# Kernel optimization log

Hardware: AMD Instinct MI355X
Metric: run time of the kernel (lower is better)

Reference implementation:

```python
import jax, jax.numpy as jnp
import numpy as np

B, C = 2, 128
FMAP_HW = [(256, 256), (128, 128), (64, 64), (32, 32)]
N_ROIS = 4000
POOL = (7, 7)
N_ANCH = 300000
N_POS = 1000          # anchors with match > 0 (class 1)
N_NEG = 200000        # anchors with match == -1
SHEM_POOLSIZE = 20
N_CLASSES = 2


def setup_inputs() -> dict:
    key = jax.random.key(0)
    ks = jax.random.split(key, 10)
    inp = {}
    for l, (h, w) in enumerate(FMAP_HW):
        inp[f"fmap{l}"] = jax.random.normal(ks[l], (B, C, h, w), dtype=jnp.float32)
    # rois: normalized (y1, x1, y2, x2, batch_ix)
    ctr = jax.random.uniform(ks[4], (N_ROIS, 2))
    sz = jax.random.uniform(ks[5], (N_ROIS, 2), minval=0.02, maxval=0.5)
    lo = jnp.clip(ctr - sz / 2, 0.0, 1.0)
    hi = jnp.clip(ctr + sz / 2, 0.0, 1.0)
    bix = jax.random.randint(ks[6], (N_ROIS, 1), 0, B).astype(jnp.float32)
    inp["rois"] = jnp.concatenate([lo, hi, bix], axis=1)
    # fixed layout for static shapes: [pos | neg | neutral]
    am = np.zeros(N_ANCH, np.int32)
    am[:N_POS] = 1
    am[N_POS:N_POS + N_NEG] = -1
    inp["anchor_matches"] = jnp.asarray(am)
    inp["class_pred_logits"] = jax.random.normal(ks[7], (N_ANCH, N_CLASSES), dtype=jnp.float32)
    inp["pred_deltas"] = jax.random.normal(ks[8], (N_ANCH, 4), dtype=jnp.float32) * 0.1
    inp["target_deltas"] = jax.random.normal(ks[9], (N_ANCH, 4), dtype=jnp.float32) * 0.1
    return inp


def _roi_align_2d(fmap, boxes, batch_ix, pool):
    """Bilinear ROI align, one sample at each bin center.
    fmap: [B,C,H,W]; boxes: [N,4] in fmap pixel coords (y1,x1,y2,x2).
    Returns [N,C,ph,pw]."""
    Hc, Wc = fmap.shape[2], fmap.shape[3]
    ph, pw = pool
    y1, x1, y2, x2 = boxes[:, 0], boxes[:, 1], boxes[:, 2], boxes[:, 3]
    bh = (y2 - y1) / ph
    bw = (x2 - x1) / pw
    iy = jnp.arange(ph, dtype=jnp.float32) + 0.5
    ix = jnp.arange(pw, dtype=jnp.float32) + 0.5
    sy = jnp.clip(y1[:, None] + bh[:, None] * iy[None, :], 0.0, Hc - 1.0)  # [N,ph]
    sx = jnp.clip(x1[:, None] + bw[:, None] * ix[None, :], 0.0, Wc - 1.0)  # [N,pw]
    y0f = jnp.floor(sy)
    x0f = jnp.floor(sx)
    y0 = y0f.astype(jnp.int32)
    x0 = x0f.astype(jnp.int32)
    y1i = jnp.minimum(y0 + 1, Hc - 1)
    x1i = jnp.minimum(x0 + 1, Wc - 1)
    wy = (sy - y0f)[:, :, None, None]  # [N,ph,1,1]
    wx = (sx - x0f)[:, None, :, None]  # [N,1,pw,1]
    b = batch_ix[:, None, None]

    def gather(yy, xx):
        # yy [N,ph], xx [N,pw] -> [N,ph,pw,C]
        return fmap[b, :, yy[:, :, None], xx[:, None, :]]

    v00 = gather(y0, x0)
    v01 = gather(y0, x1i)
    v10 = gather(y1i, x0)
    v11 = gather(y1i, x1i)
    out = (v00 * (1 - wy) * (1 - wx) + v01 * (1 - wy) * wx
           + v10 * wy * (1 - wx) + v11 * wy * wx)
    return jnp.transpose(out, (0, 3, 1, 2))


def _forward(fmaps, rois, anchor_matches, class_pred_logits, pred_deltas, target_deltas):
    boxes = rois[:, :4]
    batch_ix = rois[:, 4].astype(jnp.int32)
    h = boxes[:, 2] - boxes[:, 0]
    w = boxes[:, 3] - boxes[:, 1]
    roi_level = jnp.clip(
        jnp.round(4.0 + jnp.log2(jnp.sqrt(h * w + 1e-12))).astype(jnp.int32), 0, 3)
    boxes_sg = jax.lax.stop_gradient(boxes)  # original detaches level_boxes
    pooled = jnp.zeros((N_ROIS, C, POOL[0], POOL[1]), fmaps[0].dtype)
    for lvl, f in enumerate(fmaps):
        He, We = f.shape[2], f.shape[3]
        lb = boxes_sg * jnp.array([He, We, He, We], jnp.float32)
        pl = _roi_align_2d(f, lb, batch_ix, POOL)
        mask = (roi_level == lvl).astype(pl.dtype)[:, None, None, None]
        pooled = pooled + mask * pl  # each roi hits exactly one level; order preserved

    # ---- class loss with SHEM (layout: [:N_POS] pos, [N_POS:N_POS+N_NEG] neg) ----
    pos_logits = class_pred_logits[:N_POS]
    pos_targets = anchor_matches[:N_POS].astype(jnp.int32)
    pos_logp = jax.nn.log_softmax(pos_logits, axis=1)
    pos_loss = -jnp.mean(jnp.take_along_axis(pos_logp, pos_targets[:, None], axis=1))

    neg_logits = class_pred_logits[N_POS:N_POS + N_NEG]
    neg_bg_prob = jax.nn.softmax(neg_logits, axis=1)[:, 0]
    negative_count = N_POS  # max(1, n_pos)
    pool_n = min(negative_count * SHEM_POOLSIZE, N_NEG)
    order = jnp.argsort(neg_bg_prob)          # ascending bg prob = hardest first
    pool_idx = order[:pool_n]
    perm = jax.random.permutation(jax.random.key(1), pool_n)
    neg_ix = pool_idx[perm[:negative_count]]  # stochastic draw from hard pool
    neg_loss = -jnp.mean(jax.nn.log_softmax(neg_logits[neg_ix], axis=1)[:, 0])
    class_loss = (pos_loss + neg_loss) / 2.0

    # ---- bbox smooth-L1 on positives (beta=1, mean reduction) ----
    diff = jnp.abs(pred_deltas[:N_POS] - target_deltas[:N_POS])
    sl1 = jnp.where(diff < 1.0, 0.5 * diff * diff, diff - 0.5)
    bbox_loss = jnp.mean(sl1)
    return pooled, class_loss, bbox_loss


def reference(fmap0, fmap1, fmap2, fmap3, rois, anchor_matches,
              class_pred_logits, pred_deltas, target_deltas):
    return _forward([fmap0, fmap1, fmap2, fmap3], rois, anchor_matches,
                    class_pred_logits, pred_deltas, target_deltas)
```

## Files before the change

### kernel.cpp

```cpp
#include <hip/hip_runtime.h>
#include <hip/hip_bf16.h>
#include <cstdint>

#define NROIS  4000
#define NCH    128
#define NBINS  49
#define N_POSA 1000
#define N_NEGA 200000
#define POOLN  20000
#define HBITS_A 13
#define ABINS  8192
#define PBINS  4096
#define SUBN   4096
#define NTRBLK 2720
#define NPREP  106
#define NRANKA 512
#define NRANKP 40
#define TPAD   136

#define L0OFF 0ull
#define L1OFF 16777216ull
#define L2OFF 20971520ull
#define L3OFF 22020096ull
#define TLELEMS 22282240ull

__device__ __forceinline__ uint32_t rotl32d(uint32_t v, int r) { return (v << r) | (v >> (32-r)); }

__device__ void tf2x32(uint32_t k0, uint32_t k1, uint32_t& x0, uint32_t& x1)
{
    const uint32_t ks2 = k0 ^ k1 ^ 0x1BD11BDAu;
    const int R0[4] = {13,15,26,6};
    const int R1[4] = {17,29,16,24};
    x0 += k0; x1 += k1;
#pragma unroll
    for (int r = 0; r < 4; ++r) { x0 += x1; x1 = rotl32d(x1, R0[r]); x1 ^= x0; }
    x0 += k1;  x1 += ks2 + 1u;
#pragma unroll
    for (int r = 0; r < 4; ++r) { x0 += x1; x1 = rotl32d(x1, R1[r]); x1 ^= x0; }
    x0 += ks2; x1 += k0 + 2u;
#pragma unroll
    for (int r = 0; r < 4; ++r) { x0 += x1; x1 = rotl32d(x1, R0[r]); x1 ^= x0; }
    x0 += k0;  x1 += k1 + 3u;
#pragma unroll
    for (int r = 0; r < 4; ++r) { x0 += x1; x1 = rotl32d(x1, R1[r]); x1 ^= x0; }
    x0 += k1;  x1 += ks2 + 4u;
#pragma unroll
    for (int r = 0; r < 4; ++r) { x0 += x1; x1 = rotl32d(x1, R0[r]); x1 ^= x0; }
    x0 += ks2; x1 += k0 + 5u;
}

__device__ __forceinline__ unsigned int monobits(float x) {
    unsigned int u = __float_as_uint(x);
    return (u & 0x80000000u) ? ~u : (u | 0x80000000u);
}

__device__ __forceinline__ unsigned short f2bf(float x) {
    union { __hip_bfloat16 h; unsigned short u; } c;
    c.h = __float2bfloat16(x);
    return c.u;
}

__global__ void k_zero(unsigned int* __restrict__ h)
{
    h[blockIdx.x*256 + threadIdx.x] = 0u;
}

__global__ __launch_bounds__(256) void k_trprep(
    const float* __restrict__ f0, const float* __restrict__ f1,
    const float* __restrict__ f2, const float* __restrict__ f3,
    __hip_bfloat16* __restrict__ tl,
    unsigned long long* __restrict__ T1, unsigned long long* __restrict__ T2,
    unsigned int* __restrict__ histA,
    unsigned int* __restrict__ histP1, unsigned int* __restrict__ histP2,
    const int* __restrict__ am, const float* __restrict__ logits,
    const float* __restrict__ pd, const float* __restrict__ td,
    float* __restrict__ prt, int ntr)
{
    __shared__ __align__(16) unsigned char smraw[32768];
    const int bid = blockIdx.x;
    const int t   = threadIdx.x;

    if (bid < ntr) {
        unsigned short* s = (unsigned short*)smraw;
        const int bz = bid / 1360;
        const int r  = bid - bz*1360;
        int lvl, tile;
        if      (r < 1024) { lvl = 0; tile = r; }
        else if (r < 1280) { lvl = 1; tile = r - 1024; }
        else if (r < 1344) { lvl = 2; tile = r - 1280; }
        else               { lvl = 3; tile = r - 1344; }
        const int HW = 65536 >> (2*lvl);
        const float* in = (lvl==0) ? f0 : (lvl==1) ? f1 : (lvl==2) ? f2 : f3;
        const size_t ooff = (lvl==0) ? L0OFF : (lvl==1) ? L1OFF : (lvl==2) ? L2OFF : L3OFF;
        const int hw0 = tile * 64;
        const float4* in4 = (const float4*)(in + (size_t)bz * 128 * HW);
        const int HW4 = HW >> 2;
        const int h4b = hw0 >> 2;
#pragma unroll
        for (int k = 0; k < 8; ++k) {
            const int idx = t + k*256;
            const int c   = idx >> 4;
            const int h4  = idx & 15;
            const float4 v = in4[(size_t)c * HW4 + h4b + h4];
            const int r0 = h4 * 4;
            const int cs = c ^ ((h4 & 7) << 3);
            s[(r0+0)*TPAD + cs] = f2bf(v.x);
            s[(r0+1)*TPAD + cs] = f2bf(v.y);
            s[(r0+2)*TPAD + cs] = f2bf(v.z);
            s[(r0+3)*TPAD + cs] = f2bf(v.w);
        }
        __syncthreads();
        uint4* out4 = (uint4*)(tl + ooff + (size_t)bz * (size_t)HW * 128
                                         + (size_t)hw0 * 128);
        const int rr = t >> 4;
        const int q  = t & 15;
        const int c8 = q * 8;
#pragma unroll
        for (int m = 0; m < 4; ++m) {
            const int row = rr + m*16;
            const int sw = ((row >> 2) & 7) << 3;
            out4[row*16 + q] = *(const uint4*)&s[row*TPAD + (c8 ^ sw)];
        }
        return;
    }

    const int pbid = bid - ntr;
    if (pbid < 40) {
        unsigned int* buf = (unsigned int*)smraw;
        unsigned int* lh1 = buf;
        unsigned int* lh2 = buf + PBINS;
        for (int b = t; b < 2*PBINS; b += 256) buf[b] = 0u;
        __syncthreads();
        const int i = pbid*256 + t;
        if (i < POOLN/2) {
            uint32_t a0 = 0u, a1 = 2u; tf2x32(0u, 1u, a0, a1);
            uint32_t b0 = 1u, b1 = 3u; tf2x32(0u, 1u, b0, b1);
            uint32_t c0 = 0u, c1 = 2u; tf2x32(a0, b0, c0, c1);
            uint32_t d0 = 1u, d1 = 3u; tf2x32(a0, b0, d0, d1);
            uint32_t x0 = (uint32_t)i, x1 = (uint32_t)(POOLN/2 + i);
            tf2x32(a1, b1, x0, x1);
            T1[i]           = ((unsigned long long)x0 << 32) | (unsigned)i;
            T1[POOLN/2 + i] = ((unsigned long long)x1 << 32) | (unsigned)(POOLN/2 + i);
            atomicAdd(&lh1[x0 >> 20], 1u);
            atomicAdd(&lh1[x1 >> 20], 1u);
            uint32_t y0 = (uint32_t)i, y1 = (uint32_t)(POOLN/2 + i);
            tf2x32(c1, d1, y0, y1);
            T2[i]           = ((unsigned long long)y0 << 32) | (unsigned)i;
            T2[POOLN/2 + i] = ((unsigned long long)y1 << 32) | (unsigned)(POOLN/2 + i);
            atomicAdd(&lh2[y0 >> 20], 1u);
            atomicAdd(&lh2[y1 >> 20], 1u);
        }
        __syncthreads();
        for (int b = t; b < PBINS; b += 256) {
            unsigned int v = lh1[b]; if (v) atomicAdd(&histP1[b], v);
            v = lh2[b];              if (v) atomicAdd(&histP2[b], v);
        }
        return;
    }
    if (pbid < 104) {
        unsigned int* buf = (unsigned int*)smraw;
        for (int b = t; b < ABINS; b += 256) buf[b] = 0u;
        __syncthreads();
        for (int i = (pbid-40)*256 + t; i < N_NEGA; i += 64*256) {
            const float l0 = logits[(size_t)(N_POSA+i)*2+0];
            const float l1 = logits[(size_t)(N_POSA+i)*2+1];
            atomicAdd(&buf[monobits(l0 - l1) >> (32-HBITS_A)], 1u);
        }
        __syncthreads();
        for (int b = t; b < ABINS; b += 256) {
            const unsigned int v = buf[b];
            if (v) atomicAdd(&histA[b], v);
        }
        return;
    }
    float* red = (float*)smraw;
    float s = 0.0f;
    if (pbid == 104) {
        for (int i = t; i < N_POSA; i += 256) {
            const int tgt = am[i];
            const float l0 = logits[(size_t)i*2+0], l1 = logits[(size_t)i*2+1];
            const float m = fmaxf(l0, l1);
            const float lse = logf(expf(l0-m) + expf(l1-m));
            const float lt = (tgt == 0) ? l0 : l1;
            s += (lt - m) - lse;
        }
    } else {
        for (int i = t; i < N_POSA*4; i += 256) {
            const float d = fabsf(pd[i] - td[i]);
            s += (d < 1.0f) ? 0.5f*d*d : d - 0.5f;
        }
    }
    red[t] = s;
    __syncthreads();
    for (int off = 128; off > 0; off >>= 1) {
        if (t < off) red[t] += red[t+off];
        __syncthreads();
    }
    if (t == 0) prt[pbid - 104] = red[0];
}

__device__ void scan_one256(const unsigned int* __restrict__ hist,
                            unsigned int* __restrict__ base,
                            unsigned int* __restrict__ basem,
                            int n, unsigned int* lds)
{
    const int t = threadIdx.x;
    const int chunk = n >> 8;
    unsigned int s = 0;
    for (int k = 0; k < chunk; ++k) s += hist[t*chunk + k];
    lds[t] = s;
    __syncthreads();
    for (int off = 1; off < 256; off <<= 1) {
        unsigned int v = (t >= off) ? lds[t-off] : 0u;
        __syncthreads();
        lds[t] += v;
        __syncthreads();
    }
    unsigned int run = (t == 0) ? 0u : lds[t-1];
    for (int k = 0; k < chunk; ++k) {
        base[t*chunk+k] = run; basem[t*chunk+k] = run;
        run += hist[t*chunk+k];
    }
    if (t == 255) { base[n] = run; basem[n] = run; }
    __syncthreads();
}

__device__ void scan_all(const unsigned int* histA, const unsigned int* histP1,
                         const unsigned int* histP2,
                         unsigned int* baseA,  unsigned int* baseAm,
                         unsigned int* baseP1, unsigned int* baseP1m,
                         unsigned int* baseP2, unsigned int* baseP2m,
                         unsigned int* sel, unsigned int* lds)
{
    scan_one256(histA, baseA, baseAm, ABINS, lds);
    scan_one256(histP1, baseP1, baseP1m, PBINS, lds);
    scan_one256(histP2, baseP2, baseP2m, PBINS, lds);
    const int t = threadIdx.x;
    const int chunk = ABINS >> 8;
    for (int k = 0; k < chunk; ++k) {
        const int bin = t*chunk + k;
        if (baseA[bin] < POOLN && baseA[bin] + histA[bin] >= POOLN)
            sel[0] = (unsigned int)bin;
    }
}

__global__ __launch_bounds__(256) void k_roiscan(
    const __hip_bfloat16* __restrict__ tl, const float* __restrict__ rois,
    float* __restrict__ out,
    const unsigned int* __restrict__ histA,
    const unsigned int* __restrict__ histP1, const unsigned int* __restrict__ histP2,
    unsigned int* __restrict__ baseA,  unsigned int* __restrict__ baseAm,
    unsigned int* __restrict__ baseP1, unsigned int* __restrict__ baseP1m,
    unsigned int* __restrict__ baseP2, unsigned int* __restrict__ baseP2m,
    unsigned int* __restrict__ sel, int nroi)
{
    __shared__ int   s_a[NBINS][4];
    __shared__ float s_w[NBINS][4];
    __shared__ float s_o[NCH * NBINS];
    const int n   = blockIdx.x;
    const int tid = threadIdx.x;

    if (n >= nroi) {
        scan_all(histA, histP1, histP2, baseA, baseAm, baseP1, baseP1m,
                 baseP2, baseP2m, sel, (unsigned int*)s_o);
        return;
    }

    const float ry1 = rois[n*5+0], rx1 = rois[n*5+1];
    const float ry2 = rois[n*5+2], rx2 = rois[n*5+3];
    const int   b   = (int)rois[n*5+4];
    const float h = ry2 - ry1, w = rx2 - rx1;
    const float lraw = rintf(4.0f + log2f(sqrtf(h*w + 1e-12f)));
    int lvl = (int)lraw; lvl = lvl < 0 ? 0 : (lvl > 3 ? 3 : lvl);
    const int H = 256 >> lvl;
    const size_t lbase = (lvl==0) ? L0OFF : (lvl==1) ? L1OFF : (lvl==2) ? L2OFF : L3OFF;
    const __hip_bfloat16* bp = tl + lbase + (size_t)b * (size_t)(H*H) * NCH;

    const float Hf  = (float)H;
    const float y1p = ry1*Hf, x1p = rx1*Hf, y2p = ry2*Hf, x2p = rx2*Hf;
    const float bh = (y2p - y1p) / 7.0f, bw = (x2p - x1p) / 7.0f;

    if (tid < NBINS) {
        const int py = tid / 7, px = tid % 7;
        float sy = y1p + bh*((float)py + 0.5f);
        float sx = x1p + bw*((float)px + 0.5f);
        sy = fminf(fmaxf(sy, 0.0f), Hf - 1.0f);
        sx = fminf(fmaxf(sx, 0.0f), Hf - 1.0f);
        const float y0f = floorf(sy), x0f = floorf(sx);
        const int y0 = (int)y0f, x0 = (int)x0f;
        const int y1i = min(y0+1, H-1), x1i = min(x0+1, H-1);
        const float wy = sy - y0f, wx = sx - x0f;
        s_a[tid][0] = y0 *H + x0;
        s_a[tid][1] = y0 *H + x1i;
        s_a[tid][2] = y1i*H + x0;
        s_a[tid][3] = y1i*H + x1i;
        const float omy = 1.0f - wy, omx = 1.0f - wx;
        s_w[tid][0] = omy*omx; s_w[tid][1] = omy*wx;
        s_w[tid][2] = wy *omx; s_w[tid][3] = wy *wx;
    }
    __syncthreads();

    const int c4 = tid & 31;
    const int bg = tid >> 5;
    for (int bin = bg; bin < NBINS; bin += 8) {
        float a0 = 0.f, a1 = 0.f, a2 = 0.f, a3 = 0.f;
#pragma unroll
        for (int tap = 0; tap < 4; ++tap) {
            const uint2 v = *(const uint2*)(bp + (size_t)s_a[bin][tap] * NCH + 4*c4);
            const float wgt = s_w[bin][tap];
            a0 += __uint_as_float(v.x << 16)         * wgt;
            a1 += __uint_as_float(v.x & 0xffff0000u) * wgt;
            a2 += __uint_as_float(v.y << 16)         * wgt;
            a3 += __uint_as_float(v.y & 0xffff0000u) * wgt;
        }
        s_o[(4*c4+0)*NBINS + bin] = a0;
        s_o[(4*c4+1)*NBINS + bin] = a1;
        s_o[(4*c4+2)*NBINS + bin] = a2;
        s_o[(4*c4+3)*NBINS + bin] = a3;
    }
    __syncthreads();

    float4* outn = (float4*)(out + (size_t)n * (NCH*NBINS));
    const float4* so4 = (const float4*)s_o;
    for (int t4 = tid; t4 < (NCH*NBINS)/4; t4 += 256)
        outn[t4] = so4[t4];
}

__global__ __launch_bounds__(256) void k_roi(
    const float* __restrict__ f0, const float* __restrict__ f1,
    const float* __restrict__ f2, const float* __restrict__ f3,
    const float* __restrict__ rois, float* __restrict__ out)
{
    __shared__ int   s_a[NBINS][4];
    __shared__ float s_w[NBINS][4];
    const int n   = blockIdx.x;
    const int tid = threadIdx.x;

    const float ry1 = rois[n*5+0], rx1 = rois[n*5+1];
    const float ry2 = rois[n*5+2], rx2 = rois[n*5+3];
    const int   b   = (int)rois[n*5+4];
    const float h = ry2 - ry1, w = rx2 - rx1;
    const float lraw = rintf(4.0f + log2f(sqrtf(h*w + 1e-12f)));
    int lvl = (int)lraw; lvl = lvl < 0 ? 0 : (lvl > 3 ? 3 : lvl);
    const int H = 256 >> lvl;
    const float* f = (lvl==0) ? f0 : (lvl==1) ? f1 : (lvl==2) ? f2 : f3;

    const float Hf  = (float)H;
    const float y1p = ry1*Hf, x1p = rx1*Hf, y2p = ry2*Hf, x2p = rx2*Hf;
    const float bh = (y2p - y1p) / 7.0f, bw = (x2p - x1p) / 7.0f;

    if (tid < NBINS) {
        const int py = tid / 7, px = tid % 7;
        float sy = y1p + bh*((float)py + 0.5f);
        float sx = x1p + bw*((float)px + 0.5f);
        sy = fminf(fmaxf(sy, 0.0f), Hf - 1.0f);
        sx = fminf(fmaxf(sx, 0.0f), Hf - 1.0f);
        const float y0f = floorf(sy), x0f = floorf(sx);
        const int y0 = (int)y0f, x0 = (int)x0f;
        const int y1i = min(y0+1, H-1), x1i = min(x0+1, H-1);
        const float wy = sy - y0f, wx = sx - x0f;
        s_a[tid][0] = y0 *H + x0;
        s_a[tid][1] = y0 *H + x1i;
        s_a[tid][2] = y1i*H + x0;
        s_a[tid][3] = y1i*H + x1i;
        const float omy = 1.0f - wy, omx = 1.0f - wx;
        s_w[tid][0] = omy*omx; s_w[tid][1] = omy*wx;
        s_w[tid][2] = wy *omx; s_w[tid][3] = wy *wx;
    }
    __syncthreads();

    const int hw = H*H;
    const float* basep = f + (size_t)b * NCH * hw;
    float* outn = out + (size_t)n * (NCH*NBINS);
    for (int t = tid; t < NCH*NBINS; t += 256) {
        const int c   = t / NBINS;
        const int bin = t - c*NBINS;
        const float* p = basep + (size_t)c * hw;
        outn[t] = p[s_a[bin][0]]*s_w[bin][0] + p[s_a[bin][1]]*s_w[bin][1]
                + p[s_a[bin][2]]*s_w[bin][2] + p[s_a[bin][3]]*s_w[bin][3];
    }
}

__global__ __launch_bounds__(256) void k_scatter(
    const float* __restrict__ logits,
    const unsigned long long* __restrict__ T1, const unsigned long long* __restrict__ T2,
    unsigned long long* __restrict__ A,
    unsigned long long* __restrict__ P1, unsigned long long* __restrict__ P2,
    unsigned int* __restrict__ baseAm, unsigned int* __restrict__ baseP1m,
    unsigned int* __restrict__ baseP2m, const unsigned int* __restrict__ sel)
{
    __shared__ unsigned int lh[ABINS];
    const int bid = blockIdx.x;
    const int t   = threadIdx.x;
    if (bid < 64) {
        for (int b = t; b < ABINS; b += 256) lh[b] = 0u;
        __syncthreads();
        const unsigned int selv = sel[0];
        const int start = bid * (N_NEGA/64);
        const int end   = start + (N_NEGA/64);
        for (int i = start + t; i < end; i += 256) {
            const float l0 = logits[(size_t)(N_POSA+i)*2+0];
            const float l1 = logits[(size_t)(N_POSA+i)*2+1];
            const unsigned int bin = monobits(l0 - l1) >> (32-HBITS_A);
            if (bin <= selv) atomicAdd(&lh[bin], 1u);
        }
        __syncthreads();
        for (int b = t; b < ABINS; b += 256) {
            const unsigned int cnt = lh[b];
            if (cnt) lh[b] = atomicAdd(&baseAm[b], cnt);
        }
        __syncthreads();
        for (int i = start + t; i < end; i += 256) {
            const float l0 = logits[(size_t)(N_POSA+i)*2+0];
            const float l1 = logits[(size_t)(N_POSA+i)*2+1];
            const unsigned int bits = monobits(l0 - l1);
            const unsigned int bin = bits >> (32-HBITS_A);
            if (bin <= selv) {
                const unsigned int pos = atomicAdd(&lh[bin], 1u);
                A[pos] = ((unsigned long long)bits << 32) | (unsigned)i;
            }
        }
        return;
    }
    const int i = (bid - 64)*256 + t;
    if (i < POOLN) {
        const unsigned long long k1 = T1[i];
        const unsigned int p1 = atomicAdd(&baseP1m[(unsigned)(k1 >> 52)], 1u);
        P1[p1] = k1;
        const unsigned long long k2 = T2[i];
        const unsigned int p2 = atomicAdd(&baseP2m[(unsigned)(k2 >> 52)], 1u);
        P2[p2] = k2;
    }
}

__global__ __launch_bounds__(1024) void k_rank(
    const unsigned long long* __restrict__ A,
    const unsigned long long* __restrict__ P1, const unsigned long long* __restrict__ P2,
    const unsigned int* __restrict__ baseA,
    const unsigned int* __restrict__ baseP1, const unsigned int* __restrict__ baseP2,
    const unsigned int* __restrict__ sel,
    unsigned int* __restrict__ As, unsigned int* __restrict__ P1s,
    unsigned int* __restrict__ P2s)
{
    __shared__ unsigned long long g[SUBN];
    __shared__ unsigned int h2[SUBN];
    __shared__ unsigned int h2b[SUBN];
    const int bid = blockIdx.x;
    const int t   = threadIdx.x;
    if (bid < NRANKA) {
        const unsigned int selv = sel[0];
        for (unsigned int bin = (unsigned)bid; bin <= selv; bin += NRANKA) {
            const int base = (int)baseA[bin];
            const int cnt  = (int)baseA[bin+1] - base;
            if (cnt <= 0) continue;
            if (cnt == 1) {
                if (t == 0) As[base] = (unsigned)(A[base] & 0xffffffffu);
                continue;
            }
            if (cnt <= SUBN) {
                for (int b = t; b < SUBN; b += 1024) h2[b] = 0u;
                __syncthreads();
                for (int k = t; k < cnt; k += 1024) {
                    const unsigned int sub = ((unsigned)(A[base+k] >> 32) >> 7) & (SUBN-1);
                    atomicAdd(&h2[sub], 1u);
                }
                __syncthreads();
                unsigned int c0 = h2[4*t+0], c1 = h2[4*t+1],
                             c2 = h2[4*t+2], c3 = h2[4*t+3];
                h2b[t] = c0 + c1 + c2 + c3;
                __syncthreads();
                for (int off = 1; off < 1024; off <<= 1) {
                    const unsigned int v = (t >= off) ? h2b[t-off] : 0u;
                    __syncthreads();
                    h2b[t] += v;
                    __syncthreads();
                }
                unsigned int run = (t == 0) ? 0u : h2b[t-1];
                __syncthreads();
                h2[4*t+0] = run; h2b[4*t+0] = run; run += c0;
                h2[4*t+1] = run; h2b[4*t+1] = run; run += c1;
                h2[4*t+2] = run; h2b[4*t+2] = run; run += c2;
                h2[4*t+3] = run; h2b[4*t+3] = run; run += c3;
                __syncthreads();
                for (int k = t; k < cnt; k += 1024) {
                    const unsigned long long key = A[base+k];
                    const unsigned int sub = ((unsigned)(key >> 32) >> 7) & (SUBN-1);
                    const unsigned int p = atomicAdd(&h2[sub], 1u);
                    g[p] = key;
                }
                __syncthreads();
                for (int p = t; p < cnt; p += 1024) {
                    const unsigned long long key = g[p];
                    const unsigned int sub = ((unsigned)(key >> 32) >> 7) & (SUBN-1);
                    const int b0 = (int)h2b[sub], e0 = (int)h2[sub];
                    int r = b0;
                    for (int q = b0; q < e0; ++q) r += (g[q] < key) ? 1 : 0;
                    As[base + r] = (unsigned)(key & 0xffffffffu);
                }
                __syncthreads();
            } else {
                for (int k = t; k < cnt; k += 1024) {
                    const unsigned long long key = A[base+k];
                    int rank = 0;
                    for (int j = 0; j < cnt; ++j) rank += (A[base+j] < key) ? 1 : 0;
                    As[base + rank] = (unsigned)(key & 0xffffffffu);
                }
            }
        }
        return;
    }
    const int gg = (bid - NRANKA)*1024 + t;
    if (gg < POOLN) {
        const unsigned long long key = P1[gg];
        const unsigned int bin = (unsigned)(key >> 52);
        const int b0 = (int)baseP1[bin], b1 = (int)baseP1[bin+1];
        int rank = 0;
        for (int j = b0; j < b1; ++j) rank += (P1[j] < key) ? 1 : 0;
        P1s[b0 + rank] = (unsigned)(key & 0xffffffffu);
    } else if (gg < 2*POOLN) {
        const int e = gg - POOLN;
        const unsigned long long key = P2[e];
        const unsigned int bin = (unsigned)(key >> 52);
        const int b0 = (int)baseP2[bin], b1 = (int)baseP2[bin+1];
        int rank = 0;
        for (int j = b0; j < b1; ++j) rank += (P2[j] < key) ? 1 : 0;
        P2s[b0 + rank] = (unsigned)(key & 0xffffffffu);
    }
}

__global__ __launch_bounds__(256) void k_final(
    const float* __restrict__ logits, const unsigned int* __restrict__ As,
    const unsigned int* __restrict__ P1s, const unsigned int* __restrict__ P2s,
    const float* __restrict__ partial, float* __restrict__ out2)
{
    __shared__ float red[256];
    const int t = threadIdx.x;
    float s = 0.0f;
    for (int j = t; j < N_POSA; j += 256) {
        const unsigned int i2 = P2s[j];
        const unsigned int r  = P1s[i2];
        const unsigned int i  = As[r];
        const float l0 = logits[(size_t)(N_POSA+i)*2+0];
        const float l1 = logits[(size_t)(N_POSA+i)*2+1];
        const float m = fmaxf(l0, l1);
        s += (l0 - m) - logf(expf(l0-m) + expf(l1-m));
    }
    red[t] = s;
    __syncthreads();
    for (int off = 128; off > 0; off >>= 1) {
        if (t < off) red[t] += red[t+off];
        __syncthreads();
    }
    if (t == 0) {
        const float neg_loss = -red[0] / (float)N_POSA;
        const float pos_loss = -partial[0] / (float)N_POSA;
        out2[0] = 0.5f * (pos_loss + neg_loss);
        out2[1] = partial[1] / (float)(N_POSA*4);
    }
}

extern "C" void kernel_launch(void* const* d_in, const int* in_sizes, int n_in,
                              void* d_out, int out_size, void* d_ws, size_t ws_size,
                              hipStream_t stream)
{
    const float* f0     = (const float*)d_in[0];
    const float* f1     = (const float*)d_in[1];
    const float* f2     = (const float*)d_in[2];
    const float* f3     = (const float*)d_in[3];
    const float* rois   = (const float*)d_in[4];
    const int*   am     = (const int*)  d_in[5];
    const float* logits = (const float*)d_in[6];
    const float* pd     = (const float*)d_in[7];
    const float* td     = (const float*)d_in[8];
    float* out = (float*)d_out;

    char* ws = (char*)d_ws;
    unsigned long long* A      = (unsigned long long*)(ws);
    unsigned long long* T1     = (unsigned long long*)(ws +  262144);
    unsigned long long* T2     = (unsigned long long*)(ws +  422144);
    unsigned long long* P1     = (unsigned long long*)(ws +  582144);
    unsigned long long* P2     = (unsigned long long*)(ws +  742144);
    unsigned int*       histA  = (unsigned int*)      (ws +  902144);
    unsigned int*       histP1 = (unsigned int*)      (ws +  934912);
    unsigned int*       histP2 = (unsigned int*)      (ws +  951296);
    unsigned int*       baseA  = (unsigned int*)      (ws +  967680);
    unsigned int*       baseAm = (unsigned int*)      (ws + 1000512);
    unsigned int*       baseP1 = (unsigned int*)      (ws + 1033344);
    unsigned int*       baseP1m= (unsigned int*)      (ws + 1049792);
    unsigned int*       baseP2 = (unsigned int*)      (ws + 1066240);
    unsigned int*       baseP2m= (unsigned int*)      (ws + 1082688);
    unsigned int*       sel    = (unsigned int*)      (ws + 1099136);
    float*              prt    = (float*)             (ws + 1099200);
    __hip_bfloat16*     tl     = (__hip_bfloat16*)    (ws + 1099264);
    unsigned int*       As     = (unsigned int*)T1;
    unsigned int*       P1s    = (unsigned int*)T2;
    unsigned int*       P2s    = (unsigned int*)((char*)T2 + 80000);
    const size_t NEED = 1099264ull + TLELEMS * 2ull;
    const bool use_cl = (ws_size >= NEED);

    k_zero<<<64, 256, 0, stream>>>(histA);

    if (use_cl) {
        k_trprep<<<NTRBLK + NPREP, 256, 0, stream>>>(f0, f1, f2, f3, tl,
                                                     T1, T2, histA, histP1, histP2,
                                                     am, logits, pd, td, prt, NTRBLK);
        k_roiscan<<<NROIS + 1, 256, 0, stream>>>(tl, rois, out,
                                                 histA, histP1, histP2,
                                                 baseA, baseAm, baseP1, baseP1m,
                                                 baseP2, baseP2m, sel, NROIS);
    } else {
        k_trprep<<<NPREP, 256, 0, stream>>>(f0, f1, f2, f3, tl,
                                            T1, T2, histA, histP1, histP2,
                                            am, logits, pd, td, prt, 0);
        k_roi<<<NROIS, 256, 0, stream>>>(f0, f1, f2, f3, rois, out);
        k_roiscan<<<1, 256, 0, stream>>>(tl, rois, out,
                                         histA, histP1, histP2,
                                         baseA, baseAm, baseP1, baseP1m,
                                         baseP2, baseP2m, sel, 0);
    }

    k_scatter<<<64 + (POOLN+255)/256, 256, 0, stream>>>(logits, T1, T2, A, P1, P2,
                                                        baseAm, baseP1m, baseP2m, sel);

    k_rank<<<NRANKA + NRANKP, 1024, 0, stream>>>(A, P1, P2, baseA, baseP1, baseP2,
                                                 sel, As, P1s, P2s);

    k_final<<<1, 256, 0, stream>>>(logits, As, P1s, P2s, prt,
                                   out + (size_t)NROIS*NCH*NBINS);
}
```

Baseline: 102.8 us.

## Fuse scatter into ROI/scan kernel with per-block local prefix scans

Merges the separate scatter kernel into the ROI-align/scan launch. Each scatter block recomputes the histogram prefix sums and selection bin locally, then reserves slots through zeroed reservation counters instead of waiting for a global scan. This removes one kernel launch and the dependency on the single scan block, so the scatter can run alongside the ROI blocks. In exchange, every scatter block repeats the scans, and packing local counts into 16-bit LDS fields raises shared-memory and atomic complexity.

```diff
diff --git a/kernel.cpp b/kernel.cpp
--- a/kernel.cpp
+++ b/kernel.cpp
@@ -17,6 +17,7 @@
 #define NRANKA 512
 #define NRANKP 40
 #define TPAD   136
+#define NSC    145
 
 #define L0OFF 0ull
 #define L1OFF 16777216ull
@@ -60,9 +61,15 @@
     return c.u;
 }
 
-__global__ void k_zero(unsigned int* __restrict__ h)
-{
-    h[blockIdx.x*256 + threadIdx.x] = 0u;
+__global__ void k_zero(unsigned int* __restrict__ h, unsigned int* __restrict__ rA,
+                       unsigned int* __restrict__ rP1, unsigned int* __restrict__ rP2)
+{
+    const int b = blockIdx.x;
+    const int i = b*256 + threadIdx.x;
+    if      (b <  64) h[i] = 0u;
+    else if (b <  96) rA[i - 64*256] = 0u;
+    else if (b < 112) rP1[i - 96*256] = 0u;
+    else              rP2[i - 112*256] = 0u;
 }
 
 __global__ __launch_bounds__(256) void k_trprep(
@@ -200,9 +207,7 @@
 }
 
 __device__ void scan_one256(const unsigned int* __restrict__ hist,
-                            unsigned int* __restrict__ base,
-                            unsigned int* __restrict__ basem,
-                            int n, unsigned int* lds)
+                            unsigned int* __restrict__ base, int n, unsigned int* lds)
 {
     const int t = threadIdx.x;
     const int chunk = n >> 8;
@@ -218,53 +223,21 @@
     }
     unsigned int run = (t == 0) ? 0u : lds[t-1];
     for (int k = 0; k < chunk; ++k) {
-        base[t*chunk+k] = run; basem[t*chunk+k] = run;
+        base[t*chunk+k] = run;
         run += hist[t*chunk+k];
     }
-    if (t == 255) { base[n] = run; basem[n] = run; }
+    if (t == 255) base[n] = run;
     __syncthreads();
 }
 
-__device__ void scan_all(const unsigned int* histA, const unsigned int* histP1,
-                         const unsigned int* histP2,
-                         unsigned int* baseA,  unsigned int* baseAm,
-                         unsigned int* baseP1, unsigned int* baseP1m,
-                         unsigned int* baseP2, unsigned int* baseP2m,
-                         unsigned int* sel, unsigned int* lds)
-{
-    scan_one256(histA, baseA, baseAm, ABINS, lds);
-    scan_one256(histP1, baseP1, baseP1m, PBINS, lds);
-    scan_one256(histP2, baseP2, baseP2m, PBINS, lds);
-    const int t = threadIdx.x;
-    const int chunk = ABINS >> 8;
-    for (int k = 0; k < chunk; ++k) {
-        const int bin = t*chunk + k;
-        if (baseA[bin] < POOLN && baseA[bin] + histA[bin] >= POOLN)
-            sel[0] = (unsigned int)bin;
-    }
-}
-
-__global__ __launch_bounds__(256) void k_roiscan(
-    const __hip_bfloat16* __restrict__ tl, const float* __restrict__ rois,
-    float* __restrict__ out,
-    const unsigned int* __restrict__ histA,
-    const unsigned int* __restrict__ histP1, const unsigned int* __restrict__ histP2,
-    unsigned int* __restrict__ baseA,  unsigned int* __restrict__ baseAm,
-    unsigned int* __restrict__ baseP1, unsigned int* __restrict__ baseP1m,
-    unsigned int* __restrict__ baseP2, unsigned int* __restrict__ baseP2m,
-    unsigned int* __restrict__ sel, int nroi)
-{
-    __shared__ int   s_a[NBINS][4];
-    __shared__ float s_w[NBINS][4];
-    __shared__ float s_o[NCH * NBINS];
-    const int n   = blockIdx.x;
+__device__ void do_roi(int n, const __hip_bfloat16* __restrict__ tl,
+                       const float* __restrict__ rois, float* __restrict__ out,
+                       unsigned char* smraw)
+{
+    int   (*s_a)[4] = (int(*)[4])smraw;
+    float (*s_w)[4] = (float(*)[4])(smraw + 784);
+    float* s_o      = (float*)(smraw + 1568);
     const int tid = threadIdx.x;
-
-    if (n >= nroi) {
-        scan_all(histA, histP1, histP2, baseA, baseAm, baseP1, baseP1m,
-                 baseP2, baseP2m, sel, (unsigned int*)s_o);
-        return;
-    }
 
     const float ry1 = rois[n*5+0], rx1 = rois[n*5+1];
     const float ry2 = rois[n*5+2], rx2 = rois[n*5+3];
@@ -326,6 +299,149 @@
         outn[t4] = so4[t4];
 }
 
+__global__ __launch_bounds__(256) void k_stage3(
+    const __hip_bfloat16* __restrict__ tl, const float* __restrict__ rois,
+    float* __restrict__ out, const float* __restrict__ logits,
+    const unsigned long long* __restrict__ T1, const unsigned long long* __restrict__ T2,
+    unsigned long long* __restrict__ A,
+    unsigned long long* __restrict__ P1, unsigned long long* __restrict__ P2,
+    const unsigned int* __restrict__ histA,
+    const unsigned int* __restrict__ histP1, const unsigned int* __restrict__ histP2,
+    unsigned int* __restrict__ baseA, unsigned int* __restrict__ baseP1,
+    unsigned int* __restrict__ baseP2,
+    unsigned int* __restrict__ resvA, unsigned int* __restrict__ resvP1,
+    unsigned int* __restrict__ resvP2,
+    unsigned int* __restrict__ sel, int rcnt)
+{
+    __shared__ __align__(16) unsigned char smraw[26656];
+    const int bid = blockIdx.x;
+    const int t   = threadIdx.x;
+    if (bid < rcnt) { do_roi(bid, tl, rois, out, smraw); return; }
+
+    const int sbid = bid - rcnt;
+    if (sbid == 0) {
+        unsigned int* lds = (unsigned int*)smraw;
+        scan_one256(histA, baseA, ABINS, lds);
+        scan_one256(histP1, baseP1, PBINS, lds);
+        scan_one256(histP2, baseP2, PBINS, lds);
+        const int chunk = ABINS >> 8;
+        for (int k = 0; k < chunk; ++k) {
+            const int bin = t*chunk + k;
+            if (baseA[bin] < POOLN && baseA[bin] + histA[bin] >= POOLN)
+                sel[0] = (unsigned int)bin;
+        }
+        return;
+    }
+    if (sbid <= 64) {
+        const int sa = sbid - 1;
+        unsigned int* lh   = (unsigned int*)smraw;
+        unsigned int* temp = (unsigned int*)(smraw + 16384);
+        unsigned int* svl  = (unsigned int*)(smraw + 17408);
+        for (int b = t; b < ABINS/2; b += 256) lh[b] = 0u;
+        unsigned int s = 0;
+        for (int k = 0; k < 32; ++k) s += histA[t*32 + k];
+        temp[t] = s;
+        __syncthreads();
+        for (int off = 1; off < 256; off <<= 1) {
+            const unsigned int v = (t >= off) ? temp[t-off] : 0u;
+            __syncthreads();
+            temp[t] += v;
+            __syncthreads();
+        }
+        unsigned int run = (t == 0) ? 0u : temp[t-1];
+        for (int k = 0; k < 32; ++k) {
+            const int b = t*32 + k;
+            const unsigned int hv = histA[b];
+            if (run < POOLN && run + hv >= POOLN) svl[0] = (unsigned int)b;
+            run += hv;
+        }
+        __syncthreads();
+        const unsigned int selv = svl[0];
+        const int start = sa * (N_NEGA/64);
+        const int end   = start + (N_NEGA/64);
+        for (int i = start + t; i < end; i += 256) {
+            const float l0 = logits[(size_t)(N_POSA+i)*2+0];
+            const float l1 = logits[(size_t)(N_POSA+i)*2+1];
+            const unsigned int bin = monobits(l0 - l1) >> (32-HBITS_A);
+            if (bin <= selv) atomicAdd(&lh[bin >> 1], 1u << ((bin & 1) << 4));
+        }
+        __syncthreads();
+        run = (t == 0) ? 0u : temp[t-1];
+        for (int k = 0; k < 32; k += 2) {
+            const int b0 = t*32 + k;
+            const unsigned int packed = lh[b0 >> 1];
+            const unsigned int c0 = packed & 0xFFFFu, c1 = packed >> 16;
+            unsigned int n0 = 0u, n1 = 0u;
+            if (c0) n0 = run + atomicAdd(&resvA[b0], c0);
+            run += histA[b0];
+            if (c1) n1 = run + atomicAdd(&resvA[b0+1], c1);
+            run += histA[b0+1];
+            lh[b0 >> 1] = n0 | (n1 << 16);
+        }
+        __syncthreads();
+        for (int i = start + t; i < end; i += 256) {
+            const float l0 = logits[(size_t)(N_POSA+i)*2+0];
+            const float l1 = logits[(size_t)(N_POSA+i)*2+1];
+            const unsigned int bits = monobits(l0 - l1);
+            const unsigned int bin = bits >> (32-HBITS_A);
+            if (bin <= selv) {
+                const unsigned int sh  = (bin & 1) << 4;
+                const unsigned int old = atomicAdd(&lh[bin >> 1], 1u << sh);
+                const unsigned int pos = (old >> sh) & 0xFFFFu;
+                A[pos] = ((unsigned long long)bits << 32) | (unsigned)i;
+            }
+        }
+        return;
+    }
+    {
+        const int sp = sbid - 65;
+        unsigned short* b1   = (unsigned short*)smraw;
+        unsigned short* b2   = (unsigned short*)(smraw + 8192);
+        unsigned int*   temp = (unsigned int*)(smraw + 16384);
+        unsigned int s = 0;
+        for (int k = 0; k < 16; ++k) s += histP1[t*16 + k];
+        temp[t] = s;
+        __syncthreads();
+        for (int off = 1; off < 256; off <<= 1) {
+            const unsigned int v = (t >= off) ? temp[t-off] : 0u;
+            __syncthreads(); temp[t] += v; __syncthreads();
+        }
+        unsigned int run = (t == 0) ? 0u : temp[t-1];
+        for (int k = 0; k < 16; ++k) {
+            const int b = t*16 + k;
+            b1[b] = (unsigned short)run;
+            run += histP1[b];
+        }
+        __syncthreads();
+        s = 0;
+        for (int k = 0; k < 16; ++k) s += histP2[t*16 + k];
+        temp[t] = s;
+        __syncthreads();
+        for (int off = 1; off < 256; off <<= 1) {
+            const unsigned int v = (t >= off) ? temp[t-off] : 0u;
+            __syncthreads(); temp[t] += v; __syncthreads();
+        }
+        run = (t == 0) ? 0u : temp[t-1];
+        for (int k = 0; k < 16; ++k) {
+            const int b = t*16 + k;
+            b2[b] = (unsigned short)run;
+            run += histP2[b];
+        }
+        __syncthreads();
+        const int i = sp*256 + t;
+        if (i < POOLN) {
+            const unsigned long long k1 = T1[i];
+            const unsigned int bn1 = (unsigned)(k1 >> 52);
+            const unsigned int p1 = (unsigned)b1[bn1] + atomicAdd(&resvP1[bn1], 1u);
+            P1[p1] = k1;
+            const unsigned long long k2 = T2[i];
+            const unsigned int bn2 = (unsigned)(k2 >> 52);
+            const unsigned int p2 = (unsigned)b2[bn2] + atomicAdd(&resvP2[bn2], 1u);
+            P2[p2] = k2;
+        }
+    }
+}
+
 __global__ __launch_bounds__(256) void k_roi(
     const float* __restrict__ f0, const float* __restrict__ f1,
     const float* __restrict__ f2, const float* __restrict__ f3,
@@ -378,58 +494,6 @@
         const float* p = basep + (size_t)c * hw;
         outn[t] = p[s_a[bin][0]]*s_w[bin][0] + p[s_a[bin][1]]*s_w[bin][1]
                 + p[s_a[bin][2]]*s_w[bin][2] + p[s_a[bin][3]]*s_w[bin][3];
-    }
-}
-
-__global__ __launch_bounds__(256) void k_scatter(
-    const float* __restrict__ logits,
-    const unsigned long long* __restrict__ T1, const unsigned long long* __restrict__ T2,
-    unsigned long long* __restrict__ A,
-    unsigned long long* __restrict__ P1, unsigned long long* __restrict__ P2,
-    unsigned int* __restrict__ baseAm, unsigned int* __restrict__ baseP1m,
-    unsigned int* __restrict__ baseP2m, const unsigned int* __restrict__ sel)
-{
-    __shared__ unsigned int lh[ABINS];
-    const int bid = blockIdx.x;
-    const int t   = threadIdx.x;
-    if (bid < 64) {
-        for (int b = t; b < ABINS; b += 256) lh[b] = 0u;
-        __syncthreads();
-        const unsigned int selv = sel[0];
-        const int start = bid * (N_NEGA/64);
-        const int end   = start + (N_NEGA/64);
-        for (int i = start + t; i < end; i += 256) {
-            const float l0 = logits[(size_t)(N_POSA+i)*2+0];
-            const float l1 = logits[(size_t)(N_POSA+i)*2+1];
-            const unsigned int bin = monobits(l0 - l1) >> (32-HBITS_A);
-            if (bin <= selv) atomicAdd(&lh[bin], 1u);
-        }
-        __syncthreads();
-        for (int b = t; b < ABINS; b += 256) {
-            const unsigned int cnt = lh[b];
-            if (cnt) lh[b] = atomicAdd(&baseAm[b], cnt);
-        }
-        __syncthreads();
-        for (int i = start + t; i < end; i += 256) {
-            const float l0 = logits[(size_t)(N_POSA+i)*2+0];
-            const float l1 = logits[(size_t)(N_POSA+i)*2+1];
-            const unsigned int bits = monobits(l0 - l1);
-            const unsigned int bin = bits >> (32-HBITS_A);
-            if (bin <= selv) {
-                const unsigned int pos = atomicAdd(&lh[bin], 1u);
-                A[pos] = ((unsigned long long)bits << 32) | (unsigned)i;
-            }
-        }
-        return;
-    }
-    const int i = (bid - 64)*256 + t;
-    if (i < POOLN) {
-        const unsigned long long k1 = T1[i];
-        const unsigned int p1 = atomicAdd(&baseP1m[(unsigned)(k1 >> 52)], 1u);
-        P1[p1] = k1;
-        const unsigned long long k2 = T2[i];
-        const unsigned int p2 = atomicAdd(&baseP2m[(unsigned)(k2 >> 52)], 1u);
-        P2[p2] = k2;
     }
 }
 
@@ -584,11 +648,11 @@
     unsigned int*       histP1 = (unsigned int*)      (ws +  934912);
     unsigned int*       histP2 = (unsigned int*)      (ws +  951296);
     unsigned int*       baseA  = (unsigned int*)      (ws +  967680);
-    unsigned int*       baseAm = (unsigned int*)      (ws + 1000512);
+    unsigned int*       resvA  = (unsigned int*)      (ws + 1000512);
     unsigned int*       baseP1 = (unsigned int*)      (ws + 1033344);
-    unsigned int*       baseP1m= (unsigned int*)      (ws + 1049792);
+    unsigned int*       resvP1 = (unsigned int*)      (ws + 1049792);
     unsigned int*       baseP2 = (unsigned int*)      (ws + 1066240);
-    unsigned int*       baseP2m= (unsigned int*)      (ws + 1082688);
+    unsigned int*       resvP2 = (unsigned int*)      (ws + 1082688);
     unsigned int*       sel    = (unsigned int*)      (ws + 1099136);
     float*              prt    = (float*)             (ws + 1099200);
     __hip_bfloat16*     tl     = (__hip_bfloat16*)    (ws + 1099264);
@@ -597,30 +661,22 @@
     unsigned int*       P2s    = (unsigned int*)((char*)T2 + 80000);
     const size_t NEED = 1099264ull + TLELEMS * 2ull;
     const bool use_cl = (ws_size >= NEED);
-
-    k_zero<<<64, 256, 0, stream>>>(histA);
-
-    if (use_cl) {
-        k_trprep<<<NTRBLK + NPREP, 256, 0, stream>>>(f0, f1, f2, f3, tl,
-                                                     T1, T2, histA, histP1, histP2,
-                                                     am, logits, pd, td, prt, NTRBLK);
-        k_roiscan<<<NROIS + 1, 256, 0, stream>>>(tl, rois, out,
-                                                 histA, histP1, histP2,
-                                                 baseA, baseAm, baseP1, baseP1m,
-                                                 baseP2, baseP2m, sel, NROIS);
-    } else {
-        k_trprep<<<NPREP, 256, 0, stream>>>(f0, f1, f2, f3, tl,
-                                            T1, T2, histA, histP1, histP2,
-                                            am, logits, pd, td, prt, 0);
+    const int rcnt = use_cl ? NROIS : 0;
+
+    k_zero<<<128, 256, 0, stream>>>(histA, resvA, resvP1, resvP2);
+
+    k_trprep<<<(use_cl ? NTRBLK : 0) + NPREP, 256, 0, stream>>>(
+        f0, f1, f2, f3, tl, T1, T2, histA, histP1, histP2,
+        am, logits, pd, td, prt, use_cl ? NTRBLK : 0);
+
+    if (!use_cl)
         k_roi<<<NROIS, 256, 0, stream>>>(f0, f1, f2, f3, rois, out);
-        k_roiscan<<<1, 256, 0, stream>>>(tl, rois, out,
-                                         histA, histP1, histP2,
-                                         baseA, baseAm, baseP1, baseP1m,
-                                         baseP2, baseP2m, sel, 0);
-    }
-
-    k_scatter<<<64 + (POOLN+255)/256, 256, 0, stream>>>(logits, T1, T2, A, P1, P2,
-                                                        baseAm, baseP1m, baseP2m, sel);
+
+    k_stage3<<<rcnt + 144, 256, 0, stream>>>(tl, rois, out, logits,
+                                             T1, T2, A, P1, P2,
+                                             histA, histP1, histP2,
+                                             baseA, baseP1, baseP2,
+                                             resvA, resvP1, resvP2, sel, rcnt);
 
     k_rank<<<NRANKA + NRANKP, 1024, 0, stream>>>(A, P1, P2, baseA, baseP1, baseP2,
                                                  sel, As, P1s, P2s);
```

Result: faster. 100.4 us (-2.4%).
